# Kernel optimization log

Measured on AMD Instinct MI355X. Metric: run time of the kernel, lower is better.

The kernel has to match this reference:

```python
import jax, jax.numpy as jnp
import numpy as np

N_NODES = 100000
N_EDGES = 1600000
IN_FEATS = 3
HID = 150
OUT = 64


def setup_inputs() -> dict:
    key = jax.random.key(0)
    ks = jax.random.split(key, 8)
    return {
        "x": jax.random.normal(ks[0], (N_NODES, IN_FEATS), dtype=jnp.float32),
        "src": jax.random.randint(ks[1], (N_EDGES,), 0, N_NODES, dtype=jnp.int32),
        "dst": jax.random.randint(ks[2], (N_EDGES,), 0, N_NODES, dtype=jnp.int32),
        "W1_self": jax.random.normal(ks[3], (IN_FEATS, HID), dtype=jnp.float32) / np.sqrt(IN_FEATS),
        "W1_neigh": jax.random.normal(ks[4], (IN_FEATS, HID), dtype=jnp.float32) / np.sqrt(IN_FEATS),
        "b1": jnp.zeros((HID,), dtype=jnp.float32),
        "W2_self": jax.random.normal(ks[5], (HID, OUT), dtype=jnp.float32) / np.sqrt(HID),
        "W2_neigh": jax.random.normal(ks[6], (HID, OUT), dtype=jnp.float32) / np.sqrt(HID),
        "b2": jnp.zeros((OUT,), dtype=jnp.float32),
    }


def _sage_conv(x, src, dst, W_self, W_neigh, b, n_nodes):
    # gather source features along edges, mean-reduce onto destinations
    msg = x[src]  # [E, F]
    agg = jax.ops.segment_sum(msg, dst, num_segments=n_nodes)  # [N, F]
    deg = jax.ops.segment_sum(jnp.ones((src.shape[0],), dtype=x.dtype), dst,
                              num_segments=n_nodes)
    h_neigh = agg / jnp.maximum(deg, 1.0)[:, None]
    return x @ W_self + h_neigh @ W_neigh + b


def reference(x, src, dst, W1_self, W1_neigh, b1, W2_self, W2_neigh, b2):
    n = x.shape[0]
    h = _sage_conv(x, src, dst, W1_self, W1_neigh, b1, n)
    h = jax.nn.relu(h)
    return _sage_conv(h, src, dst, W2_self, W2_neigh, b2, n)
```

## Files before the change

### kernel.cpp

```cpp
#include <hip/hip_runtime.h>

#define N_NODES 100000
#define N_PAD 100032
#define N_EDGES 1600000
#define HID 150
#define KPAD 160
#define HROW 168
#define OUTF 64
#define BSH 9
#define BUKN 512
#define NBUK ((N_NODES + BUKN - 1) / BUKN)
#define CAP 10240
#define TILE 4096
#define NTILE ((N_EDGES + TILE - 1) / TILE)

typedef short bf16x8 __attribute__((ext_vector_type(8)));
typedef float f32x4 __attribute__((ext_vector_type(4)));

__device__ __forceinline__ unsigned short f2bf(float f) {
    union { float f; unsigned u; } v; v.f = f;
    unsigned r = (v.u + 0x7FFFu + ((v.u >> 16) & 1u)) >> 16;
    return (unsigned short)r;
}

__device__ __forceinline__ float bf2f(unsigned short b) {
    union { unsigned u; float f; } v;
    v.u = ((unsigned)b) << 16;
    return v.f;
}

__global__ __launch_bounds__(256) void k_init(const float* __restrict__ W1s,
                                              const float* __restrict__ W1n,
                                              const float* __restrict__ b1,
                                              const float* __restrict__ W2s,
                                              const float* __restrict__ W2n,
                                              unsigned short* __restrict__ W1B,
                                              unsigned short* __restrict__ W2T,
                                              int* __restrict__ bukcnt) {
    int tid = threadIdx.x;
    if (tid < NBUK) bukcnt[tid] = 0;
    for (int idx = tid; idx < 10 * 64 * 8; idx += 256) {
        int t = idx >> 9;
        int r = idx & 511;
        int ln = r >> 3;
        int j = r & 7;
        int q = ln >> 4;
        int c = t * 16 + (ln & 15);
        float v = 0.0f;
        if (q == 0 && c < HID) {
            if (j < 3)       v = W1s[j * HID + c];
            else if (j == 3) v = b1[c];
            else if (j < 7)  v = W1n[(j - 4) * HID + c];
        }
        W1B[idx] = f2bf(v);
    }
    for (int idx = tid; idx < 128 * KPAD; idx += 256) {
        int c = idx / KPAD, k = idx - c * KPAD;
        float v = 0.0f;
        if (k < HID) v = (c < 64) ? W2s[k * 64 + c] : W2n[k * 64 + (c - 64)];
        W2T[idx] = f2bf(v);
    }
}

__global__ __launch_bounds__(256) void k_part(const float* __restrict__ x,
                                              float4* __restrict__ x4,
                                              const int* __restrict__ src,
                                              const int* __restrict__ dst,
                                              int* __restrict__ bukcnt,
                                              unsigned int* __restrict__ pairbuf) {
    __shared__ int cnt[NBUK];
    __shared__ int gbase[NBUK];
    int tid = threadIdx.x;
    int idx = blockIdx.x * 256 + tid;
    if (idx < N_NODES)
        x4[idx] = make_float4(x[idx * 3 + 0], x[idx * 3 + 1], x[idx * 3 + 2], 0.0f);

    int e0 = blockIdx.x * TILE;
    int n = min(TILE, N_EDGES - e0);

    for (int i = tid; i < NBUK; i += 256) cnt[i] = 0;
    __syncthreads();

    int myb[16];
    int mypos[16];
    unsigned int myv[16];
    #pragma unroll
    for (int j = 0; j < 16; ++j) {
        int ei = tid + j * 256;
        myb[j] = -1;
        if (ei < n) {
            int s = src[e0 + ei];
            int d = dst[e0 + ei];
            int b = d >> BSH;
            myb[j] = b;
            myv[j] = ((unsigned int)(d & (BUKN - 1)) << 17) | (unsigned int)s;
            mypos[j] = atomicAdd(&cnt[b], 1);
        }
    }
    __syncthreads();

    if (tid < NBUK) {
        int c = cnt[tid];
        gbase[tid] = c ? (tid * CAP + atomicAdd(&bukcnt[tid], c)) : 0;
    }
    __syncthreads();

    #pragma unroll
    for (int j = 0; j < 16; ++j) {
        if (myb[j] >= 0)
            pairbuf[gbase[myb[j]] + mypos[j]] = myv[j];
    }
}

__global__ __launch_bounds__(512) void k_fine(const int* __restrict__ bukcnt,
                                              const unsigned int* __restrict__ pairbuf,
                                              int2* __restrict__ rows,
                                              float* __restrict__ invd,
                                              int* __restrict__ csr_src) {
    __shared__ int deg[BUKN];
    __shared__ int sc[BUKN];
    int tid = threadIdx.x;
    int b = blockIdx.x;
    int n0 = b << BSH;
    int lo = b * CAP;
    int hi = lo + bukcnt[b];

    deg[tid] = 0;
    __syncthreads();
    for (int i = lo + tid; i < hi; i += 512)
        atomicAdd(&deg[pairbuf[i] >> 17], 1);
    __syncthreads();

    int d = deg[tid];
    sc[tid] = d;
    __syncthreads();
    for (int o = 1; o < 512; o <<= 1) {
        int a = sc[tid];
        int ap = (tid >= o) ? sc[tid - o] : 0;
        __syncthreads();
        sc[tid] = a + ap;
        __syncthreads();
    }
    int r = lo + sc[tid] - d;
    int node = n0 + tid;
    if (node < N_NODES) {
        rows[node] = make_int2(r, r + d);
        invd[node] = 1.0f / fmaxf((float)d, 1.0f);
    }
    __syncthreads();
    deg[tid] = r;
    __syncthreads();
    for (int i = lo + tid; i < hi; i += 512) {
        unsigned int v = pairbuf[i];
        int dl = v >> 17;
        int ofs = atomicAdd(&deg[dl], 1);
        csr_src[ofs] = (int)(v & 0x1FFFF);
    }
}

__global__ void k_agg1(const int2* __restrict__ rows, const int* __restrict__ csr_src,
                       const float4* __restrict__ x4, const float* __restrict__ invd,
                       float4* __restrict__ hn4) {
    int wid = (blockIdx.x * blockDim.x + threadIdx.x) >> 6;
    int lane = threadIdx.x & 63;
    int n = wid * 16 + (lane >> 2);
    if (n >= N_NODES) return;
    int sub = lane & 3;
    int2 re = rows[n];
    float s0 = 0.f, s1 = 0.f, s2 = 0.f;
    for (int i = re.x + sub; i < re.y; i += 4) {
        float4 v = x4[csr_src[i]];
        s0 += v.x; s1 += v.y; s2 += v.z;
    }
    s0 += __shfl_xor(s0, 1, 64); s0 += __shfl_xor(s0, 2, 64);
    s1 += __shfl_xor(s1, 1, 64); s1 += __shfl_xor(s1, 2, 64);
    s2 += __shfl_xor(s2, 1, 64); s2 += __shfl_xor(s2, 2, 64);
    if (sub == 0) {
        float id = invd[n];
        hn4[n] = make_float4(s0 * id, s1 * id, s2 * id, 0.0f);
    }
}

__global__ __launch_bounds__(256, 2) void k_gemm(
        const float4* __restrict__ x4, const float4* __restrict__ hn4,
        const unsigned short* __restrict__ W1B,
        const unsigned short* __restrict__ W2T,
        const float* __restrict__ b2,
        unsigned short* __restrict__ ob) {
    __shared__ unsigned short shH[64 * HROW];
    const int n0 = blockIdx.x * 64;
    const int tid = threadIdx.x;
    const int lane = tid & 63;
    const int w = tid >> 6;
    const int c16 = lane & 15;
    const int quad = lane >> 4;
    const int nb = w * 16;

    bf16x8 a8 = (bf16x8){0, 0, 0, 0, 0, 0, 0, 0};
    if (quad == 0) {
        int node = n0 + nb + c16;
        float4 xs = make_float4(0.f, 0.f, 0.f, 0.f);
        float4 xn = make_float4(0.f, 0.f, 0.f, 0.f);
        if (node < N_NODES) { xs = x4[node]; xn = hn4[node]; }
        union { unsigned int u[4]; bf16x8 v; } t;
        t.u[0] = (unsigned int)f2bf(xs.x) | ((unsigned int)f2bf(xs.y) << 16);
        t.u[1] = (unsigned int)f2bf(xs.z) | (0x3F80u << 16);
        t.u[2] = (unsigned int)f2bf(xn.x) | ((unsigned int)f2bf(xn.y) << 16);
        t.u[3] = (unsigned int)f2bf(xn.z);
        a8 = t.v;
    }

    #pragma unroll
    for (int t10 = 0; t10 < 10; ++t10) {
        bf16x8 b = *(const bf16x8*)&W1B[(t10 * 64 + lane) * 8];
        f32x4 z = __builtin_amdgcn_mfma_f32_16x16x32_bf16(
                      a8, b, (f32x4){0.f, 0.f, 0.f, 0.f}, 0, 0, 0);
        #pragma unroll
        for (int i = 0; i < 4; ++i) {
            float h = fmaxf(z[i], 0.0f);
            shH[(nb + quad * 4 + i) * HROW + t10 * 16 + c16] = f2bf(h);
        }
    }

    const int ko = quad * 8;
    f32x4 acc[8];
    #pragma unroll
    for (int t = 0; t < 8; ++t) acc[t] = (f32x4){0.f, 0.f, 0.f, 0.f};

    #pragma unroll
    for (int ks = 0; ks < 5; ++ks) {
        int k0 = ks * 32;
        bf16x8 a = *(const bf16x8*)&shH[(nb + c16) * HROW + k0 + ko];
        #pragma unroll
        for (int t = 0; t < 8; ++t) {
            bf16x8 b = *(const bf16x8*)&W2T[(t * 16 + c16) * KPAD + k0 + ko];
            acc[t] = __builtin_amdgcn_mfma_f32_16x16x32_bf16(a, b, acc[t], 0, 0, 0);
        }
    }

    const int rbase = n0 + nb + quad * 4;
    #pragma unroll
    for (int t = 0; t < 8; ++t) {
        int cc = t * 16 + c16;
        float badd = (t < 4) ? b2[cc] : 0.0f;
        #pragma unroll
        for (int i = 0; i < 4; ++i) {
            int node = rbase + i;
            if (node < N_NODES) ob[(size_t)node * 128 + cc] = f2bf(acc[t][i] + badd);
        }
    }
}

__global__ __launch_bounds__(256) void k_pull(const int2* __restrict__ rows,
                                              const int* __restrict__ csr_src,
                                              const unsigned short* __restrict__ ob,
                                              const float* __restrict__ invd,
                                              float* __restrict__ out) {
    int wid = blockIdx.x * 4 + (threadIdx.x >> 6);
    int lane = threadIdx.x & 63;
    int g = lane >> 3;
    int t = lane & 7;
    int n = wid * 8 + g;
    if (n >= N_NODES) return;
    int2 re = rows[n];

    float acc[8];
    #pragma unroll
    for (int q = 0; q < 8; ++q) acc[q] = 0.0f;

    #pragma unroll 4
    for (int i = re.x; i < re.y; ++i) {
        int s = csr_src[i];
        bf16x8 v = *(const bf16x8*)&ob[(size_t)s * 128 + 64 + t * 8];
        #pragma unroll
        for (int q = 0; q < 8; ++q) acc[q] += bf2f((unsigned short)v[q]);
    }

    float id = invd[n];
    bf16x8 sv = *(const bf16x8*)&ob[(size_t)n * 128 + t * 8];
    f32x4 o0, o1;
    o0[0] = bf2f((unsigned short)sv[0]) + acc[0] * id;
    o0[1] = bf2f((unsigned short)sv[1]) + acc[1] * id;
    o0[2] = bf2f((unsigned short)sv[2]) + acc[2] * id;
    o0[3] = bf2f((unsigned short)sv[3]) + acc[3] * id;
    o1[0] = bf2f((unsigned short)sv[4]) + acc[4] * id;
    o1[1] = bf2f((unsigned short)sv[5]) + acc[5] * id;
    o1[2] = bf2f((unsigned short)sv[6]) + acc[6] * id;
    o1[3] = bf2f((unsigned short)sv[7]) + acc[7] * id;
    *(f32x4*)&out[(size_t)n * OUTF + t * 8]     = o0;
    *(f32x4*)&out[(size_t)n * OUTF + t * 8 + 4] = o1;
}


static inline size_t al256(size_t v) { return (v + 255) & ~(size_t)255; }

extern "C" void kernel_launch(void* const* d_in, const int* in_sizes, int n_in,
                              void* d_out, int out_size, void* d_ws, size_t ws_size,
                              hipStream_t stream) {
    const float* x   = (const float*)d_in[0];
    const int*   src = (const int*)d_in[1];
    const int*   dst = (const int*)d_in[2];
    const float* W1s = (const float*)d_in[3];
    const float* W1n = (const float*)d_in[4];
    const float* b1  = (const float*)d_in[5];
    const float* W2s = (const float*)d_in[6];
    const float* W2n = (const float*)d_in[7];
    const float* b2  = (const float*)d_in[8];
    float* out = (float*)d_out;

    char* ws = (char*)d_ws;
    size_t off = 0;
    int2*  rows      = (int2*)(ws + off); off += al256((size_t)N_NODES * 8);
    int*   csr_src   = (int*)(ws + off); off += al256((size_t)NBUK * CAP * 4);
    float* invd      = (float*)(ws + off); off += al256((size_t)N_NODES * 4);
    unsigned short* ob = (unsigned short*)(ws + off); off += al256((size_t)N_NODES * 128 * 2);
    float4* x4       = (float4*)(ws + off); off += al256((size_t)N_NODES * 16);
    float4* hn4      = (float4*)(ws + off); off += al256((size_t)N_NODES * 16);
    unsigned int* pairbuf = (unsigned int*)(ws + off); off += al256((size_t)NBUK * CAP * 4);
    int*   bukcnt    = (int*)(ws + off); off += al256((size_t)NBUK * 4);
    unsigned short* W1B = (unsigned short*)(ws + off); off += al256((size_t)10 * 64 * 8 * 2);
    unsigned short* W2T = (unsigned short*)(ws + off); off += al256((size_t)128 * KPAD * 2);

    k_init<<<1, 256, 0, stream>>>(W1s, W1n, b1, W2s, W2n, W1B, W2T, bukcnt);
    k_part<<<NTILE, 256, 0, stream>>>(x, x4, src, dst, bukcnt, pairbuf);
    k_fine<<<NBUK, 512, 0, stream>>>(bukcnt, pairbuf, rows, invd, csr_src);
    {
        int waves = (N_NODES + 15) / 16;
        int blocks = (waves * 64 + 255) / 256;
        k_agg1<<<blocks, 256, 0, stream>>>(rows, csr_src, x4, invd, hn4);
    }
    {
        int blocks = N_PAD / 64;
        k_gemm<<<blocks, 256, 0, stream>>>(x4, hn4, W1B, W2T, b2, ob);
    }
    {
        int blocks = (N_NODES + 31) / 32;
        k_pull<<<blocks, 256, 0, stream>>>(rows, csr_src, ob, invd, out);
    }
}
```

Measured before the change: 135.6 us.

## Fuse layer-1 neighbor aggregation into GEMM kernel and weight prep into partition

Removes the separate k_agg1 kernel: each wave of k_gemm now gathers and mean-reduces the 3-feature neighbor sums for its own 16 nodes, then broadcasts them via shuffles into the MFMA A-operand. This eliminates the hn4 intermediate buffer round-trip and one launch. The weight bf16 conversion moves from the single-block init kernel into the first blocks of k_part, leaving a tiny init kernel that only zeroes bucket counts. The gather latency now sits inside the GEMM kernel, whose occupancy is limited by launch bounds and shared memory, so the irregular loads may be hidden less well.

New measurement: 115.8 us. -14.6%, faster.

```diff
diff --git a/kernel.cpp b/kernel.cpp
--- a/kernel.cpp
+++ b/kernel.cpp
@@ -13,6 +13,8 @@
 #define CAP 10240
 #define TILE 4096
 #define NTILE ((N_EDGES + TILE - 1) / TILE)
+#define W1B_N (10 * 64 * 8)
+#define W2T_N (128 * KPAD)
 
 typedef short bf16x8 __attribute__((ext_vector_type(8)));
 typedef float f32x4 __attribute__((ext_vector_type(4)));
@@ -29,17 +31,30 @@
     return v.f;
 }
 
-__global__ __launch_bounds__(256) void k_init(const float* __restrict__ W1s,
+__global__ __launch_bounds__(256) void k_init0(int* __restrict__ bukcnt) {
+    int tid = threadIdx.x;
+    if (tid < NBUK) bukcnt[tid] = 0;
+}
+
+__global__ __launch_bounds__(256) void k_part(const float* __restrict__ x,
+                                              float4* __restrict__ x4,
+                                              const int* __restrict__ src,
+                                              const int* __restrict__ dst,
+                                              int* __restrict__ bukcnt,
+                                              unsigned int* __restrict__ pairbuf,
+                                              const float* __restrict__ W1s,
                                               const float* __restrict__ W1n,
                                               const float* __restrict__ b1,
                                               const float* __restrict__ W2s,
                                               const float* __restrict__ W2n,
                                               unsigned short* __restrict__ W1B,
-                                              unsigned short* __restrict__ W2T,
-                                              int* __restrict__ bukcnt) {
+                                              unsigned short* __restrict__ W2T) {
+    __shared__ int cnt[NBUK];
+    __shared__ int gbase[NBUK];
     int tid = threadIdx.x;
-    if (tid < NBUK) bukcnt[tid] = 0;
-    for (int idx = tid; idx < 10 * 64 * 8; idx += 256) {
+    int idx = blockIdx.x * 256 + tid;
+
+    if (idx < W1B_N) {
         int t = idx >> 9;
         int r = idx & 511;
         int ln = r >> 3;
@@ -53,25 +68,14 @@
             else if (j < 7)  v = W1n[(j - 4) * HID + c];
         }
         W1B[idx] = f2bf(v);
-    }
-    for (int idx = tid; idx < 128 * KPAD; idx += 256) {
-        int c = idx / KPAD, k = idx - c * KPAD;
+    } else if (idx < W1B_N + W2T_N) {
+        int i2 = idx - W1B_N;
+        int c = i2 / KPAD, k = i2 - c * KPAD;
         float v = 0.0f;
         if (k < HID) v = (c < 64) ? W2s[k * 64 + c] : W2n[k * 64 + (c - 64)];
-        W2T[idx] = f2bf(v);
-    }
-}
-
-__global__ __launch_bounds__(256) void k_part(const float* __restrict__ x,
-                                              float4* __restrict__ x4,
-                                              const int* __restrict__ src,
-                                              const int* __restrict__ dst,
-                                              int* __restrict__ bukcnt,
-                                              unsigned int* __restrict__ pairbuf) {
-    __shared__ int cnt[NBUK];
-    __shared__ int gbase[NBUK];
-    int tid = threadIdx.x;
-    int idx = blockIdx.x * 256 + tid;
+        W2T[i2] = f2bf(v);
+    }
+
     if (idx < N_NODES)
         x4[idx] = make_float4(x[idx * 3 + 0], x[idx * 3 + 1], x[idx * 3 + 2], 0.0f);
 
@@ -158,31 +162,11 @@
     }
 }
 
-__global__ void k_agg1(const int2* __restrict__ rows, const int* __restrict__ csr_src,
-                       const float4* __restrict__ x4, const float* __restrict__ invd,
-                       float4* __restrict__ hn4) {
-    int wid = (blockIdx.x * blockDim.x + threadIdx.x) >> 6;
-    int lane = threadIdx.x & 63;
-    int n = wid * 16 + (lane >> 2);
-    if (n >= N_NODES) return;
-    int sub = lane & 3;
-    int2 re = rows[n];
-    float s0 = 0.f, s1 = 0.f, s2 = 0.f;
-    for (int i = re.x + sub; i < re.y; i += 4) {
-        float4 v = x4[csr_src[i]];
-        s0 += v.x; s1 += v.y; s2 += v.z;
-    }
-    s0 += __shfl_xor(s0, 1, 64); s0 += __shfl_xor(s0, 2, 64);
-    s1 += __shfl_xor(s1, 1, 64); s1 += __shfl_xor(s1, 2, 64);
-    s2 += __shfl_xor(s2, 1, 64); s2 += __shfl_xor(s2, 2, 64);
-    if (sub == 0) {
-        float id = invd[n];
-        hn4[n] = make_float4(s0 * id, s1 * id, s2 * id, 0.0f);
-    }
-}
-
 __global__ __launch_bounds__(256, 2) void k_gemm(
-        const float4* __restrict__ x4, const float4* __restrict__ hn4,
+        const float4* __restrict__ x4,
+        const int2* __restrict__ rows,
+        const int* __restrict__ csr_src,
+        const float* __restrict__ invd,
         const unsigned short* __restrict__ W1B,
         const unsigned short* __restrict__ W2T,
         const float* __restrict__ b2,
@@ -196,17 +180,38 @@
     const int quad = lane >> 4;
     const int nb = w * 16;
 
+    float s0 = 0.f, s1 = 0.f, s2 = 0.f;
+    {
+        int j = lane >> 2;
+        int sub = lane & 3;
+        int nj = n0 + nb + j;
+        if (nj < N_NODES) {
+            int2 re = rows[nj];
+            for (int i = re.x + sub; i < re.y; i += 4) {
+                float4 v = x4[csr_src[i]];
+                s0 += v.x; s1 += v.y; s2 += v.z;
+            }
+        }
+        s0 += __shfl_xor(s0, 1, 64); s0 += __shfl_xor(s0, 2, 64);
+        s1 += __shfl_xor(s1, 1, 64); s1 += __shfl_xor(s1, 2, 64);
+        s2 += __shfl_xor(s2, 1, 64); s2 += __shfl_xor(s2, 2, 64);
+        float id = (nj < N_NODES) ? invd[nj] : 0.0f;
+        s0 *= id; s1 *= id; s2 *= id;
+    }
+    float xn0 = __shfl(s0, c16 * 4, 64);
+    float xn1 = __shfl(s1, c16 * 4, 64);
+    float xn2 = __shfl(s2, c16 * 4, 64);
+
     bf16x8 a8 = (bf16x8){0, 0, 0, 0, 0, 0, 0, 0};
     if (quad == 0) {
         int node = n0 + nb + c16;
         float4 xs = make_float4(0.f, 0.f, 0.f, 0.f);
-        float4 xn = make_float4(0.f, 0.f, 0.f, 0.f);
-        if (node < N_NODES) { xs = x4[node]; xn = hn4[node]; }
+        if (node < N_NODES) xs = x4[node];
         union { unsigned int u[4]; bf16x8 v; } t;
         t.u[0] = (unsigned int)f2bf(xs.x) | ((unsigned int)f2bf(xs.y) << 16);
         t.u[1] = (unsigned int)f2bf(xs.z) | (0x3F80u << 16);
-        t.u[2] = (unsigned int)f2bf(xn.x) | ((unsigned int)f2bf(xn.y) << 16);
-        t.u[3] = (unsigned int)f2bf(xn.z);
+        t.u[2] = (unsigned int)f2bf(xn0) | ((unsigned int)f2bf(xn1) << 16);
+        t.u[3] = (unsigned int)f2bf(xn2);
         a8 = t.v;
     }
 
@@ -315,23 +320,18 @@
     float* invd      = (float*)(ws + off); off += al256((size_t)N_NODES * 4);
     unsigned short* ob = (unsigned short*)(ws + off); off += al256((size_t)N_NODES * 128 * 2);
     float4* x4       = (float4*)(ws + off); off += al256((size_t)N_NODES * 16);
-    float4* hn4      = (float4*)(ws + off); off += al256((size_t)N_NODES * 16);
     unsigned int* pairbuf = (unsigned int*)(ws + off); off += al256((size_t)NBUK * CAP * 4);
     int*   bukcnt    = (int*)(ws + off); off += al256((size_t)NBUK * 4);
-    unsigned short* W1B = (unsigned short*)(ws + off); off += al256((size_t)10 * 64 * 8 * 2);
-    unsigned short* W2T = (unsigned short*)(ws + off); off += al256((size_t)128 * KPAD * 2);
-
-    k_init<<<1, 256, 0, stream>>>(W1s, W1n, b1, W2s, W2n, W1B, W2T, bukcnt);
-    k_part<<<NTILE, 256, 0, stream>>>(x, x4, src, dst, bukcnt, pairbuf);
+    unsigned short* W1B = (unsigned short*)(ws + off); off += al256((size_t)W1B_N * 2);
+    unsigned short* W2T = (unsigned short*)(ws + off); off += al256((size_t)W2T_N * 2);
+
+    k_init0<<<1, 256, 0, stream>>>(bukcnt);
+    k_part<<<NTILE, 256, 0, stream>>>(x, x4, src, dst, bukcnt, pairbuf,
+                                      W1s, W1n, b1, W2s, W2n, W1B, W2T);
     k_fine<<<NBUK, 512, 0, stream>>>(bukcnt, pairbuf, rows, invd, csr_src);
     {
-        int waves = (N_NODES + 15) / 16;
-        int blocks = (waves * 64 + 255) / 256;
-        k_agg1<<<blocks, 256, 0, stream>>>(rows, csr_src, x4, invd, hn4);
-    }
-    {
         int blocks = N_PAD / 64;
-        k_gemm<<<blocks, 256, 0, stream>>>(x4, hn4, W1B, W2T, b2, ob);
+        k_gemm<<<blocks, 256, 0, stream>>>(x4, rows, csr_src, invd, W1B, W2T, b2, ob);
     }
     {
         int blocks = (N_NODES + 31) / 32;
```
